# Kernel tuning notes

Measured on AMD Instinct MI355X. Metric: run time of the kernel, lower is better.

The kernel has to match this reference:

```python
import jax, jax.numpy as jnp
import numpy as np

N, M, C = 32768, 8192, 128
K = 3            # number of interpolation neighbors (PointNet++/RepSurf FP)
EPS_BN = 1e-5    # torch BatchNorm1d default eps
EPS_D = 1e-8     # RepSurf dist_recip eps


def setup_inputs() -> dict:
    key = jax.random.key(0)
    ks = jax.random.split(key, 16)
    s = 0.05
    inp = {
        "pos1": jax.random.normal(ks[0], (N, 3), jnp.float32),
        "pos2": jax.random.normal(ks[1], (M, 3), jnp.float32),
        "feat2": jax.random.normal(ks[2], (M, C), jnp.float32),
    }
    # MLP stack [128,128,128]: Linear + BatchNorm1d (gamma/beta) per layer
    for i in range(3):
        inp[f"W{i}"] = jax.random.normal(ks[3 + i], (C, C), jnp.float32) * s
        inp[f"b{i}"] = jnp.zeros((C,), jnp.float32)
        inp[f"g{i}"] = jnp.ones((C,), jnp.float32)
        inp[f"be{i}"] = jnp.zeros((C,), jnp.float32)
    return inp


def _lin_bn_relu(x, W, b, g, be):
    # Linear -> BatchNorm1d (training-mode batch stats, biased var) -> ReLU
    y = x @ W.T + b
    m = y.mean(axis=0)
    v = y.var(axis=0)
    return jax.nn.relu((y - m) * jax.lax.rsqrt(v + EPS_BN) * g + be)


def reference(pos1, pos2, feat2, W0, b0, g0, be0, W1, b1, g1, be1, W2, b2, g2, be2):
    # squared pairwise distances [N, M] (memory-bound: 1 GB fp32)
    d = ((pos1 ** 2).sum(-1, keepdims=True)
         + (pos2 ** 2).sum(-1)[None, :]
         - 2.0 * (pos1 @ pos2.T))
    neg_d, idx = jax.lax.top_k(-d, K)          # 3 nearest neighbors
    dk = jnp.maximum(-neg_d, 0.0)              # [N, K] squared dists
    w = 1.0 / (dk + EPS_D)
    w = w / w.sum(-1, keepdims=True)           # inverse-distance weights
    # gather neighbor features and interpolate: [N, K, C] -> [N, C]
    interp = jnp.einsum('nkc,nk->nc', feat2[idx], w)
    x = _lin_bn_relu(interp, W0, b0, g0, be0)
    x = _lin_bn_relu(x, W1, b1, g1, be1)
    x = _lin_bn_relu(x, W2, b2, g2, be2)
    return x
```

## Files before the change

### kernel.cpp

```cpp
#include <hip/hip_runtime.h>
#include <hip/hip_fp16.h>
#include <math.h>

#define NQ 32768
#define MC 8192
#define CC 128
#define EPS_BN 1e-5f
#define EPS_D  1e-8

#define DBL_BIG 1e300
#define IDX_BIG 0x7fffffff

#define QB  64
#define TB  256
#define NTIL 256
#define KMASK 0xFFFFE000u
#define IMASK 0x1FFFu
#define NSURV 24
#define KNN_B ((NQ / QB) * 2)
#define GEMM_B (NQ / 64)
#define NGRP 8

typedef __attribute__((ext_vector_type(8))) short bf16x8;
typedef __attribute__((ext_vector_type(8))) _Float16 half8;
typedef __attribute__((ext_vector_type(4))) float floatx4;
typedef unsigned short ushort_t;

__device__ __forceinline__ unsigned bf16pair(float a, float b) {
    unsigned ua = __float_as_uint(a); ua = (ua + 0x7FFFu + ((ua >> 16) & 1u)) >> 16;
    unsigned ub = __float_as_uint(b); ub = (ub + 0x7FFFu + ((ub >> 16) & 1u)) >> 16;
    return ua | (ub << 16);
}
__device__ __forceinline__ ushort_t bf16one(float a) {
    unsigned ua = __float_as_uint(a);
    return (ushort_t)((ua + 0x7FFFu + ((ua >> 16) & 1u)) >> 16);
}
__device__ __forceinline__ float bflo(unsigned u) { return __uint_as_float(u << 16); }
__device__ __forceinline__ float bfhi(unsigned u) { return __uint_as_float(u & 0xFFFF0000u); }

__device__ __forceinline__ void ins3(float& k0, float& k1, float& k2, float x) {
    const float n0 = fminf(k0, x);
    const float n1 = __builtin_amdgcn_fmed3f(k0, k1, x);
    const float n2 = __builtin_amdgcn_fmed3f(k1, k2, x);
    k0 = n0; k1 = n1; k2 = n2;
}

#define PK2(a, b) ((unsigned)__half_as_ushort(a) | ((unsigned)__half_as_ushort(b) << 16))

__global__ __launch_bounds__(TB) void pack_kernel(const float* __restrict__ pos2,
                                                  uint4* __restrict__ ptile) {
    const int c = blockIdx.x * TB + threadIdx.x;
    const float x = pos2[c * 3 + 0];
    const float y = pos2[c * 3 + 1];
    const float z = pos2[c * 3 + 2];
    const __half chx = __float2half(x); const float fchx = __half2float(chx);
    const __half chy = __float2half(y); const float fchy = __half2float(chy);
    const __half chz = __float2half(z); const float fchz = __half2float(chz);
    const __half clx = __float2half(x - fchx);
    const __half cly = __float2half(y - fchy);
    const __half clz = __float2half(z - fchz);
    const double X = (double)fchx + (double)__half2float(clx);
    const double Y = (double)fchy + (double)__half2float(cly);
    const double Z = (double)fchz + (double)__half2float(clz);
    const double hc = 0.5 * (X * X + Y * Y + Z * Z);
    const __half hchi = __float2half((float)hc);
    const __half hclo = __float2half((float)(hc - (double)__half2float(hchi)));
    const __half one = __float2half(1.0f);
    uint4 a0, a1;
    a0.x = PK2(chx, chy); a0.y = PK2(chz, clx); a0.z = PK2(cly, clz); a0.w = PK2(chx, chy);
    a1.x = PK2(chz, clx); a1.y = PK2(cly, clz); a1.z = PK2(hchi, hclo); a1.w = PK2(one, one);
    const int t = c >> 4, m = c & 15;
    ptile[(size_t)t * 32 + m]      = a0;
    ptile[(size_t)t * 32 + 16 + m] = a1;
}

__global__ __launch_bounds__(TB) void knn_kernel(const float* __restrict__ pos1,
                                                 const uint4* __restrict__ ptile,
                                                 unsigned* __restrict__ skeys,
                                                 const float* __restrict__ W0,
                                                 const float* __restrict__ W1,
                                                 const float* __restrict__ W2,
                                                 ushort_t* __restrict__ Wbf,
                                                 float* __restrict__ stats) {
    __shared__ __align__(16) ushort_t qext[QB][16];

    if (blockIdx.x >= KNN_B) {
        const int pb = blockIdx.x - KNN_B;
        const int f = pb * TB + threadIdx.x;
        const float* Ws[3] = {W0, W1, W2};
#pragma unroll
        for (int l = 0; l < 3; ++l) {
            const float4 v = ((const float4*)Ws[l])[f];
            unsigned* dst = (unsigned*)(Wbf + (size_t)l * CC * CC);
            dst[f * 2 + 0] = bf16pair(v.x, v.y);
            dst[f * 2 + 1] = bf16pair(v.z, v.w);
        }
        if (pb == 0)
            for (int i = threadIdx.x; i < 3 * NGRP * 256; i += TB) stats[i] = 0.f;
        return;
    }

    const int half = blockIdx.x & 1;
    const int bq   = blockIdx.x >> 1;

    if (threadIdx.x < QB) {
        const int qq = bq * QB + threadIdx.x;
        const float x = pos1[qq * 3 + 0];
        const float y = pos1[qq * 3 + 1];
        const float z = pos1[qq * 3 + 2];
        const __half phx = __float2half(x); const float fphx = __half2float(phx);
        const __half phy = __float2half(y); const float fphy = __half2float(phy);
        const __half phz = __float2half(z); const float fphz = __half2float(phz);
        const __half plx = __float2half(x - fphx);
        const __half ply = __float2half(y - fphy);
        const __half plz = __float2half(z - fphz);
        const double X = (double)fphx + (double)__half2float(plx);
        const double Y = (double)fphy + (double)__half2float(ply);
        const double Z = (double)fphz + (double)__half2float(plz);
        const double hp = 0.5 * (X * X + Y * Y + Z * Z);
        const __half hphi = __float2half((float)hp);
        const __half hplo = __float2half((float)(hp - (double)__half2float(hphi)));
        const ushort_t SG = 0x8000u;
        const ushort_t nx = (ushort_t)(__half_as_ushort(phx) ^ SG);
        const ushort_t ny = (ushort_t)(__half_as_ushort(phy) ^ SG);
        const ushort_t nz = (ushort_t)(__half_as_ushort(phz) ^ SG);
        const ushort_t mx = (ushort_t)(__half_as_ushort(plx) ^ SG);
        const ushort_t my = (ushort_t)(__half_as_ushort(ply) ^ SG);
        const ushort_t mz = (ushort_t)(__half_as_ushort(plz) ^ SG);
        const ushort_t on = __half_as_ushort(__float2half(1.0f));
        ushort_t* e = &qext[threadIdx.x][0];
        e[0] = nx; e[1] = ny; e[2] = nz; e[3] = nx; e[4]  = ny; e[5]  = nz;
        e[6] = mx; e[7] = my; e[8] = mz; e[9] = mx; e[10] = my; e[11] = mz;
        e[12] = on; e[13] = on;
        e[14] = __half_as_ushort(hphi); e[15] = __half_as_ushort(hplo);
    }
    __syncthreads();

    const int lane = threadIdx.x & 63;
    const int wv   = threadIdx.x >> 6;
    const int cc   = lane & 15;
    const int g    = lane >> 4;

    uint4 bqu = {0u, 0u, 0u, 0u};
    if (g < 2) bqu = *(const uint4*)&qext[wv * 16 + cc][g * 8];
    const half8 bqh = *(const half8*)&bqu;

    const uint4* lp = ptile + (size_t)(half * NTIL) * 32 + ((g & 1) * 16 + cc);
#define LD(t) lp[(size_t)(t) * 32]

    const float KINIT = __uint_as_float(0x7F000000u);
    float k0 = KINIT, k1 = KINIT, k2 = KINIT;
    unsigned j0 = (unsigned)(half * 4096 + g * 4 + 0);
    unsigned j1 = j0 + 1, j2 = j0 + 2, j3 = j0 + 3;
    const floatx4 zc = {0.f, 0.f, 0.f, 0.f};

#define KEYS(d) { \
        unsigned u0 = (__float_as_uint(d[0]) & KMASK) | (j0 & ~KMASK); \
        unsigned u1 = (__float_as_uint(d[1]) & KMASK) | (j1 & ~KMASK); \
        unsigned u2 = (__float_as_uint(d[2]) & KMASK) | (j2 & ~KMASK); \
        unsigned u3 = (__float_as_uint(d[3]) & KMASK) | (j3 & ~KMASK); \
        ins3(k0, k1, k2, __uint_as_float(u0)); \
        ins3(k0, k1, k2, __uint_as_float(u1)); \
        ins3(k0, k1, k2, __uint_as_float(u2)); \
        ins3(k0, k1, k2, __uint_as_float(u3)); \
        j0 += 16; j1 += 16; j2 += 16; j3 += 16; }

    uint4 afA = LD(0);
    uint4 afB = LD(1);
    for (int t = 0; t < NTIL; t += 2) {
        const uint4 nA = LD(t + 2);
        const floatx4 dA = __builtin_amdgcn_mfma_f32_16x16x32_f16(*(const half8*)&afA, bqh, zc, 0, 0, 0);
        KEYS(dA);
        const uint4 nB = LD(t + 3);
        const floatx4 dB = __builtin_amdgcn_mfma_f32_16x16x32_f16(*(const half8*)&afB, bqh, zc, 0, 0, 0);
        KEYS(dB);
        afA = nA; afB = nB;
    }
#undef LD
#undef KEYS

    {
        const int q = bq * QB + wv * 16 + cc;
        unsigned* dst = skeys + (size_t)q * NSURV + half * 12 + g * 3;
        dst[0] = __float_as_uint(k0);
        dst[1] = __float_as_uint(k1);
        dst[2] = __float_as_uint(k2);
    }
}

template <int MODE>
__global__ __launch_bounds__(256) void gemm_mfma(const void* __restrict__ Xsrc_,
                                                 const unsigned* __restrict__ skeys,
                                                 const float* __restrict__ pos1,
                                                 const float* __restrict__ pos2,
                                                 const float* __restrict__ statsIn,
                                                 const float* __restrict__ gIn,
                                                 const float* __restrict__ beIn,
                                                 const ushort_t* __restrict__ Wb,
                                                 const float* __restrict__ bias,
                                                 ushort_t* __restrict__ Y,
                                                 float* __restrict__ statsOut) {
    __shared__ __align__(16) short xa[64][136];
    __shared__ __align__(16) short wb[128][136];
    __shared__ float blk_s[CC], blk_q[CC];
    __shared__ float sc_l[CC], sh_l[CC];

    const int row0 = blockIdx.x * 64;

    if constexpr (MODE == 0) {
        const float* feat2 = (const float*)Xsrc_;
        __shared__ int   lidx[QB][3];
        __shared__ float lw[QB][3];
        {
            double* rrd = (double*)&xa[0][0];
            int*    rri = (int*)&wb[0][0];
            const int ql = threadIdx.x >> 2;
            const int pp = threadIdx.x & 3;
            const int qg = row0 + ql;
            const double qx = (double)pos1[qg * 3 + 0];
            const double qy = (double)pos1[qg * 3 + 1];
            const double qz = (double)pos1[qg * 3 + 2];
            double b0 = DBL_BIG, b1 = DBL_BIG, b2 = DBL_BIG;
            int    j0 = IDX_BIG, j1 = IDX_BIG, j2 = IDX_BIG;
            const uint2* kp = (const uint2*)(skeys + (size_t)qg * NSURV + pp * 6);
            const uint2 ka = kp[0], kb = kp[1], kc = kp[2];
            const unsigned ks[6] = {ka.x, ka.y, kb.x, kb.y, kc.x, kc.y};
#pragma unroll
            for (int u = 0; u < 6; ++u) {
                const int id = (int)(ks[u] & IMASK);
                const double x = (double)pos2[id * 3 + 0];
                const double y = (double)pos2[id * 3 + 1];
                const double z = (double)pos2[id * 3 + 2];
                const double ax = qx - x, ay = qy - y, az = qz - z;
                const double d = ax * ax + ay * ay + az * az;
                const bool l2 = (d < b2) || (d == b2 && id < j2);
                if (l2) {
                    const bool l1 = (d < b1) || (d == b1 && id < j1);
                    const bool l0 = (d < b0) || (d == b0 && id < j0);
                    b2 = l1 ? b1 : d;              j2 = l1 ? j1 : id;
                    b1 = l1 ? (l0 ? b0 : d) : b1;  j1 = l1 ? (l0 ? j0 : id) : j1;
                    b0 = l0 ? d : b0;              j0 = l0 ? id : j0;
                }
            }
            const int base = (ql * 4 + pp) * 3;
            rrd[base + 0] = b0; rri[base + 0] = j0;
            rrd[base + 1] = b1; rri[base + 1] = j1;
            rrd[base + 2] = b2; rri[base + 2] = j2;
            __syncthreads();
            if (threadIdx.x < QB) {
                const int qq = threadIdx.x;
                double c0 = DBL_BIG, c1 = DBL_BIG, c2 = DBL_BIG;
                int    i0 = IDX_BIG, i1 = IDX_BIG, i2 = IDX_BIG;
#pragma unroll
                for (int s = 0; s < 12; ++s) {
                    const double d = rrd[qq * 12 + s];
                    const int   id = rri[qq * 12 + s];
                    const bool l2 = (d < c2) || (d == c2 && id < i2);
                    if (l2) {
                        const bool l1 = (d < c1) || (d == c1 && id < i1);
                        const bool l0 = (d < c0) || (d == c0 && id < i0);
                        c2 = l1 ? c1 : d;              i2 = l1 ? i1 : id;
                        c1 = l1 ? (l0 ? c0 : d) : c1;  i1 = l1 ? (l0 ? i0 : id) : i1;
                        c0 = l0 ? d : c0;              i0 = l0 ? id : i0;
                    }
                }
                const double r0 = 1.0 / (c0 + EPS_D);
                const double r1 = 1.0 / (c1 + EPS_D);
                const double r2 = 1.0 / (c2 + EPS_D);
                const double inv = 1.0 / (r0 + r1 + r2);
                lidx[qq][0] = i0; lidx[qq][1] = i1; lidx[qq][2] = i2;
                lw[qq][0] = (float)(r0 * inv);
                lw[qq][1] = (float)(r1 * inv);
                lw[qq][2] = (float)(r2 * inv);
            }
            __syncthreads();
        }
        if (threadIdx.x < CC) { blk_s[threadIdx.x] = 0.f; blk_q[threadIdx.x] = 0.f; }
#pragma unroll
        for (int e = threadIdx.x; e < 64 * 32; e += 256) {
            const int r = e >> 5, c4 = e & 31;
            const int i0 = lidx[r][0], i1 = lidx[r][1], i2 = lidx[r][2];
            const float w0 = lw[r][0], w1 = lw[r][1], w2 = lw[r][2];
            const float4 f0 = *(const float4*)&feat2[(size_t)i0 * CC + c4 * 4];
            const float4 f1 = *(const float4*)&feat2[(size_t)i1 * CC + c4 * 4];
            const float4 f2 = *(const float4*)&feat2[(size_t)i2 * CC + c4 * 4];
            float4 v;
            v.x = w0 * f0.x + w1 * f1.x + w2 * f2.x;
            v.y = w0 * f0.y + w1 * f1.y + w2 * f2.y;
            v.z = w0 * f0.z + w1 * f1.z + w2 * f2.z;
            v.w = w0 * f0.w + w1 * f1.w + w2 * f2.w;
            unsigned* dst = (unsigned*)&xa[r][0];
            dst[c4 * 2 + 0] = bf16pair(v.x, v.y);
            dst[c4 * 2 + 1] = bf16pair(v.z, v.w);
        }
    } else {
        const ushort_t* Xbf = (const ushort_t*)Xsrc_;
        if (threadIdx.x < CC) {
            const int c = threadIdx.x;
            float s = 0.f, q = 0.f;
#pragma unroll
            for (int gr = 0; gr < NGRP; ++gr) {
                s += statsIn[gr * 256 + c];
                q += statsIn[gr * 256 + CC + c];
            }
            const float m = s * (1.f / (float)NQ);
            const float v = fmaf(-m, m, q * (1.f / (float)NQ));
            const float rstd = rsqrtf(v + EPS_BN);
            const float scl = gIn[c] * rstd;
            sc_l[c] = scl;
            sh_l[c] = fmaf(-m, scl, beIn[c]);
            blk_s[c] = 0.f; blk_q[c] = 0.f;
        }
        __syncthreads();
#pragma unroll
        for (int e = threadIdx.x; e < 64 * 16; e += 256) {
            const int r = e >> 4, c8 = e & 15;
            const uint4 u = *(const uint4*)&Xbf[(size_t)(row0 + r) * CC + c8 * 8];
            const float4 s0 = *(const float4*)&sc_l[c8 * 8];
            const float4 s1 = *(const float4*)&sc_l[c8 * 8 + 4];
            const float4 h0 = *(const float4*)&sh_l[c8 * 8];
            const float4 h1 = *(const float4*)&sh_l[c8 * 8 + 4];
            const float v0 = fmaxf(fmaf(bflo(u.x), s0.x, h0.x), 0.f);
            const float v1 = fmaxf(fmaf(bfhi(u.x), s0.y, h0.y), 0.f);
            const float v2 = fmaxf(fmaf(bflo(u.y), s0.z, h0.z), 0.f);
            const float v3 = fmaxf(fmaf(bfhi(u.y), s0.w, h0.w), 0.f);
            const float v4 = fmaxf(fmaf(bflo(u.z), s1.x, h1.x), 0.f);
            const float v5 = fmaxf(fmaf(bfhi(u.z), s1.y, h1.y), 0.f);
            const float v6 = fmaxf(fmaf(bflo(u.w), s1.z, h1.z), 0.f);
            const float v7 = fmaxf(fmaf(bfhi(u.w), s1.w, h1.w), 0.f);
            uint4 o;
            o.x = bf16pair(v0, v1); o.y = bf16pair(v2, v3);
            o.z = bf16pair(v4, v5); o.w = bf16pair(v6, v7);
            *(uint4*)&xa[r][c8 * 8] = o;
        }
    }
#pragma unroll
    for (int e = threadIdx.x; e < 128 * 16; e += 256) {
        const int co = e >> 4, seg = e & 15;
        *(float4*)&wb[co][seg * 8] = *(const float4*)&Wb[(size_t)co * CC + seg * 8];
    }
    __syncthreads();

    const int lane = threadIdx.x & 63;
    const int wv = threadIdx.x >> 6;
    const int nn = lane & 15;
    const int quad = lane >> 4;

    floatx4 acc[8] = {};

    const short* arow = &xa[wv * 16 + nn][0];
#pragma unroll
    for (int ks = 0; ks < 4; ++ks) {
        const bf16x8 a = *(const bf16x8*)(arow + ks * 32 + quad * 8);
#pragma unroll
        for (int ct = 0; ct < 8; ++ct) {
            const bf16x8 b = *(const bf16x8*)(&wb[ct * 16 + nn][0] + ks * 32 + quad * 8);
            acc[ct] = __builtin_amdgcn_mfma_f32_16x16x32_bf16(a, b, acc[ct], 0, 0, 0);
        }
    }

#pragma unroll
    for (int ct = 0; ct < 8; ++ct) {
        const float bv = bias[ct * 16 + nn];
        float s = 0.f, qv = 0.f;
#pragma unroll
        for (int r = 0; r < 4; ++r) {
            acc[ct][r] += bv;
            s += acc[ct][r];
            qv = fmaf(acc[ct][r], acc[ct][r], qv);
        }
#pragma unroll
        for (int r = 0; r < 4; ++r)
            Y[(size_t)(row0 + wv * 16 + quad * 4 + r) * CC + ct * 16 + nn] = bf16one(acc[ct][r]);
        s += __shfl_xor(s, 16, 64); s += __shfl_xor(s, 32, 64);
        qv += __shfl_xor(qv, 16, 64); qv += __shfl_xor(qv, 32, 64);
        if (quad == 0) {
            atomicAdd(&blk_s[ct * 16 + nn], s);
            atomicAdd(&blk_q[ct * 16 + nn], qv);
        }
    }
    __syncthreads();
    {
        const int ch = threadIdx.x;
        const float v = (ch < CC) ? blk_s[ch] : blk_q[ch - CC];
        atomicAdd(&statsOut[(blockIdx.x & (NGRP - 1)) * 256 + ch], v);
    }
}

__global__ __launch_bounds__(256) void bn_final(const ushort_t* __restrict__ Y,
                                                const float* __restrict__ statsIn,
                                                const float* __restrict__ g,
                                                const float* __restrict__ be,
                                                float* __restrict__ out) {
    __shared__ float sc_l[CC], sh_l[CC];
    if (threadIdx.x < CC) {
        const int c = threadIdx.x;
        float s = 0.f, q = 0.f;
#pragma unroll
        for (int gr = 0; gr < NGRP; ++gr) {
            s += statsIn[gr * 256 + c];
            q += statsIn[gr * 256 + CC + c];
        }
        const float m = s * (1.f / (float)NQ);
        const float v = fmaf(-m, m, q * (1.f / (float)NQ));
        const float rstd = rsqrtf(v + EPS_BN);
        const float scl = g[c] * rstd;
        sc_l[c] = scl;
        sh_l[c] = fmaf(-m, scl, be[c]);
    }
    __syncthreads();
    const int base = blockIdx.x * 1024 + threadIdx.x;
#pragma unroll
    for (int it = 0; it < 4; ++it) {
        const int i8 = base + it * 256;
        const int c8 = (i8 & 15) * 8;
        const uint4 u = *(const uint4*)&Y[(size_t)i8 * 8];
        const float4 s0 = *(const float4*)&sc_l[c8];
        const float4 s1 = *(const float4*)&sc_l[c8 + 4];
        const float4 h0 = *(const float4*)&sh_l[c8];
        const float4 h1 = *(const float4*)&sh_l[c8 + 4];
        float4 o0, o1;
        o0.x = fmaxf(fmaf(bflo(u.x), s0.x, h0.x), 0.f);
        o0.y = fmaxf(fmaf(bfhi(u.x), s0.y, h0.y), 0.f);
        o0.z = fmaxf(fmaf(bflo(u.y), s0.z, h0.z), 0.f);
        o0.w = fmaxf(fmaf(bfhi(u.y), s0.w, h0.w), 0.f);
        o1.x = fmaxf(fmaf(bflo(u.z), s1.x, h1.x), 0.f);
        o1.y = fmaxf(fmaf(bfhi(u.z), s1.y, h1.y), 0.f);
        o1.z = fmaxf(fmaf(bflo(u.w), s1.z, h1.z), 0.f);
        o1.w = fmaxf(fmaf(bfhi(u.w), s1.w, h1.w), 0.f);
        ((float4*)out)[i8 * 2 + 0] = o0;
        ((float4*)out)[i8 * 2 + 1] = o1;
    }
}

extern "C" void kernel_launch(void* const* d_in, const int* in_sizes, int n_in,
                              void* d_out, int out_size, void* d_ws, size_t ws_size,
                              hipStream_t stream) {
    (void)in_sizes; (void)n_in; (void)out_size; (void)ws_size;

    const float* pos1  = (const float*)d_in[0];
    const float* pos2  = (const float*)d_in[1];
    const float* feat2 = (const float*)d_in[2];
    const float* Wl[3]  = {(const float*)d_in[3], (const float*)d_in[7],  (const float*)d_in[11]};
    const float* bl[3]  = {(const float*)d_in[4], (const float*)d_in[8],  (const float*)d_in[12]};
    const float* gl[3]  = {(const float*)d_in[5], (const float*)d_in[9],  (const float*)d_in[13]};
    const float* bel[3] = {(const float*)d_in[6], (const float*)d_in[10], (const float*)d_in[14]};

    float* ws = (float*)d_ws;
    ushort_t* B0 = (ushort_t*)ws;
    ushort_t* B1 = B0 + (size_t)NQ * CC;
    unsigned* skeys = (unsigned*)(B1 + (size_t)NQ * CC);
    float* stats = (float*)(skeys + (size_t)NQ * NSURV);
    ushort_t* Wbf = (ushort_t*)(stats + 3 * NGRP * 256);
    uint4* ptile = (uint4*)(Wbf + 3 * CC * CC);

    float* st0 = stats + 0 * NGRP * 256;
    float* st1 = stats + 1 * NGRP * 256;
    float* st2 = stats + 2 * NGRP * 256;

    pack_kernel<<<MC / TB, TB, 0, stream>>>(pos2, ptile);
    knn_kernel<<<KNN_B + 16, TB, 0, stream>>>(pos1, ptile, skeys,
                                              Wl[0], Wl[1], Wl[2], Wbf, stats);
    gemm_mfma<0><<<GEMM_B, 256, 0, stream>>>(feat2, skeys, pos1, pos2,
                                             nullptr, nullptr, nullptr,
                                             Wbf + 0 * CC * CC, bl[0], B0, st0);
    gemm_mfma<1><<<GEMM_B, 256, 0, stream>>>(B0, nullptr, nullptr, nullptr,
                                             st0, gl[0], bel[0],
                                             Wbf + 1 * CC * CC, bl[1], B1, st1);
    gemm_mfma<1><<<GEMM_B, 256, 0, stream>>>(B1, nullptr, nullptr, nullptr,
                                             st1, gl[1], bel[1],
                                             Wbf + 2 * CC * CC, bl[2], B0, st2);
    bn_final<<<GEMM_B, 256, 0, stream>>>(B0, st2, gl[2], bel[2], (float*)d_out);
}
```

Measured before the change: 201.4 us.

## Switch KNN distance MFMA to 32x32x16 tiles and split candidates four ways

The brute-force KNN distance pass now uses 32x32x16 f16 MFMA instead of 16x16x32, so each wave covers 32 queries. Candidates are split into four pieces per query block, and each lane keeps four independent top-3 lists that are merged at the end. The point tile layout is rebuilt for 32-wide tiles, with zero padding added for the prefetch overrun. The survivor count per query doubles to 48, so the refinement step in the GEMM kernel reads and rechecks twice as many candidates in double precision. The aim is to raise MFMA throughput and shorten the serial insertion dependency chains, at the cost of more blocks, more survivor traffic and more refine work.

```diff
diff --git a/kernel.cpp b/kernel.cpp
--- a/kernel.cpp
+++ b/kernel.cpp
@@ -13,17 +13,19 @@
 
 #define QB  64
 #define TB  256
-#define NTIL 256
+#define PCE 2048
+#define NT  32
 #define KMASK 0xFFFFE000u
 #define IMASK 0x1FFFu
-#define NSURV 24
-#define KNN_B ((NQ / QB) * 2)
+#define NSURV 48
+#define KNN_B ((NQ / QB) * 4)
 #define GEMM_B (NQ / 64)
 #define NGRP 8
 
 typedef __attribute__((ext_vector_type(8))) short bf16x8;
 typedef __attribute__((ext_vector_type(8))) _Float16 half8;
 typedef __attribute__((ext_vector_type(4))) float floatx4;
+typedef __attribute__((ext_vector_type(16))) float floatx16;
 typedef unsigned short ushort_t;
 
 __device__ __forceinline__ unsigned bf16pair(float a, float b) {
@@ -69,9 +71,13 @@
     uint4 a0, a1;
     a0.x = PK2(chx, chy); a0.y = PK2(chz, clx); a0.z = PK2(cly, clz); a0.w = PK2(chx, chy);
     a1.x = PK2(chz, clx); a1.y = PK2(cly, clz); a1.z = PK2(hchi, hclo); a1.w = PK2(one, one);
-    const int t = c >> 4, m = c & 15;
-    ptile[(size_t)t * 32 + m]      = a0;
-    ptile[(size_t)t * 32 + 16 + m] = a1;
+    const int t = c >> 5, m = c & 31;
+    ptile[(size_t)t * 64 + m]      = a0;
+    ptile[(size_t)t * 64 + 32 + m] = a1;
+    if (blockIdx.x == 0 && threadIdx.x < 128) {
+        uint4 zf = {0u, 0u, 0u, 0u};
+        ptile[(size_t)256 * 64 + threadIdx.x] = zf;
+    }
 }
 
 __global__ __launch_bounds__(TB) void knn_kernel(const float* __restrict__ pos1,
@@ -100,8 +106,8 @@
         return;
     }
 
-    const int half = blockIdx.x & 1;
-    const int bq   = blockIdx.x >> 1;
+    const int piece = blockIdx.x & 3;
+    const int bq    = blockIdx.x >> 2;
 
     if (threadIdx.x < QB) {
         const int qq = bq * QB + threadIdx.x;
@@ -137,54 +143,69 @@
     __syncthreads();
 
     const int lane = threadIdx.x & 63;
-    const int wv   = threadIdx.x >> 6;
-    const int cc   = lane & 15;
-    const int g    = lane >> 4;
-
-    uint4 bqu = {0u, 0u, 0u, 0u};
-    if (g < 2) bqu = *(const uint4*)&qext[wv * 16 + cc][g * 8];
+    const int w    = threadIdx.x >> 6;
+    const int qt   = w >> 1;
+    const int wh   = w & 1;
+    const int col  = lane & 31;
+    const int h    = lane >> 5;
+
+    const uint4 bqu = *(const uint4*)&qext[qt * 32 + col][h * 8];
     const half8 bqh = *(const half8*)&bqu;
 
-    const uint4* lp = ptile + (size_t)(half * NTIL) * 32 + ((g & 1) * 16 + cc);
-#define LD(t) lp[(size_t)(t) * 32]
+    const int cw = piece * PCE + wh * 1024;
+    const uint4* lp = ptile + (size_t)(cw >> 5) * 64 + h * 32 + col;
+#define LD(t) lp[(size_t)(t) * 64]
 
     const float KINIT = __uint_as_float(0x7F000000u);
-    float k0 = KINIT, k1 = KINIT, k2 = KINIT;
-    unsigned j0 = (unsigned)(half * 4096 + g * 4 + 0);
-    unsigned j1 = j0 + 1, j2 = j0 + 2, j3 = j0 + 3;
-    const floatx4 zc = {0.f, 0.f, 0.f, 0.f};
-
+    float a0 = KINIT, a1 = KINIT, a2 = KINIT;
+    float b0 = KINIT, b1 = KINIT, b2 = KINIT;
+    float c0 = KINIT, c1 = KINIT, c2 = KINIT;
+    float d0 = KINIT, d1 = KINIT, d2 = KINIT;
+    unsigned ja = (unsigned)(cw + 4 * h + 0);
+    unsigned jb = (unsigned)(cw + 4 * h + 8);
+    unsigned jc = (unsigned)(cw + 4 * h + 16);
+    unsigned jd = (unsigned)(cw + 4 * h + 24);
+    const floatx16 zc = {0.f,0.f,0.f,0.f,0.f,0.f,0.f,0.f,0.f,0.f,0.f,0.f,0.f,0.f,0.f,0.f};
+
+#define KEY1(v, jj, K0, K1, K2) { \
+        const unsigned u_ = (__float_as_uint(v) & KMASK) | ((jj) & ~KMASK); \
+        ins3(K0, K1, K2, __uint_as_float(u_)); }
 #define KEYS(d) { \
-        unsigned u0 = (__float_as_uint(d[0]) & KMASK) | (j0 & ~KMASK); \
-        unsigned u1 = (__float_as_uint(d[1]) & KMASK) | (j1 & ~KMASK); \
-        unsigned u2 = (__float_as_uint(d[2]) & KMASK) | (j2 & ~KMASK); \
-        unsigned u3 = (__float_as_uint(d[3]) & KMASK) | (j3 & ~KMASK); \
-        ins3(k0, k1, k2, __uint_as_float(u0)); \
-        ins3(k0, k1, k2, __uint_as_float(u1)); \
-        ins3(k0, k1, k2, __uint_as_float(u2)); \
-        ins3(k0, k1, k2, __uint_as_float(u3)); \
-        j0 += 16; j1 += 16; j2 += 16; j3 += 16; }
-
-    uint4 afA = LD(0);
-    uint4 afB = LD(1);
-    for (int t = 0; t < NTIL; t += 2) {
-        const uint4 nA = LD(t + 2);
-        const floatx4 dA = __builtin_amdgcn_mfma_f32_16x16x32_f16(*(const half8*)&afA, bqh, zc, 0, 0, 0);
+        KEY1(d[0],  ja,     a0, a1, a2); KEY1(d[1],  ja + 1, a0, a1, a2); \
+        KEY1(d[2],  ja + 2, a0, a1, a2); KEY1(d[3],  ja + 3, a0, a1, a2); \
+        KEY1(d[4],  jb,     b0, b1, b2); KEY1(d[5],  jb + 1, b0, b1, b2); \
+        KEY1(d[6],  jb + 2, b0, b1, b2); KEY1(d[7],  jb + 3, b0, b1, b2); \
+        KEY1(d[8],  jc,     c0, c1, c2); KEY1(d[9],  jc + 1, c0, c1, c2); \
+        KEY1(d[10], jc + 2, c0, c1, c2); KEY1(d[11], jc + 3, c0, c1, c2); \
+        KEY1(d[12], jd,     d0, d1, d2); KEY1(d[13], jd + 1, d0, d1, d2); \
+        KEY1(d[14], jd + 2, d0, d1, d2); KEY1(d[15], jd + 3, d0, d1, d2); \
+        ja += 32; jb += 32; jc += 32; jd += 32; }
+
+    uint4 fA = LD(0);
+    uint4 fB = LD(1);
+    floatx16 dA = __builtin_amdgcn_mfma_f32_32x32x16_f16(*(const half8*)&fA, bqh, zc, 0, 0, 0);
+    for (int t = 0; t < NT; t += 2) {
+        fA = LD(t + 2);
+        const floatx16 dB = __builtin_amdgcn_mfma_f32_32x32x16_f16(*(const half8*)&fB, bqh, zc, 0, 0, 0);
         KEYS(dA);
-        const uint4 nB = LD(t + 3);
-        const floatx4 dB = __builtin_amdgcn_mfma_f32_16x16x32_f16(*(const half8*)&afB, bqh, zc, 0, 0, 0);
+        fB = LD(t + 3);
+        dA = __builtin_amdgcn_mfma_f32_32x32x16_f16(*(const half8*)&fA, bqh, zc, 0, 0, 0);
         KEYS(dB);
-        afA = nA; afB = nB;
     }
 #undef LD
 #undef KEYS
+#undef KEY1
+
+    ins3(a0, a1, a2, b0); ins3(a0, a1, a2, b1); ins3(a0, a1, a2, b2);
+    ins3(a0, a1, a2, c0); ins3(a0, a1, a2, c1); ins3(a0, a1, a2, c2);
+    ins3(a0, a1, a2, d0); ins3(a0, a1, a2, d1); ins3(a0, a1, a2, d2);
 
     {
-        const int q = bq * QB + wv * 16 + cc;
-        unsigned* dst = skeys + (size_t)q * NSURV + half * 12 + g * 3;
-        dst[0] = __float_as_uint(k0);
-        dst[1] = __float_as_uint(k1);
-        dst[2] = __float_as_uint(k2);
+        const int q = bq * QB + qt * 32 + col;
+        unsigned* dst = skeys + (size_t)q * NSURV + piece * 12 + wh * 6 + h * 3;
+        dst[0] = __float_as_uint(a0);
+        dst[1] = __float_as_uint(a1);
+        dst[2] = __float_as_uint(a2);
     }
 }
 
@@ -222,24 +243,27 @@
             const double qz = (double)pos1[qg * 3 + 2];
             double b0 = DBL_BIG, b1 = DBL_BIG, b2 = DBL_BIG;
             int    j0 = IDX_BIG, j1 = IDX_BIG, j2 = IDX_BIG;
-            const uint2* kp = (const uint2*)(skeys + (size_t)qg * NSURV + pp * 6);
-            const uint2 ka = kp[0], kb = kp[1], kc = kp[2];
-            const unsigned ks[6] = {ka.x, ka.y, kb.x, kb.y, kc.x, kc.y};
-#pragma unroll
-            for (int u = 0; u < 6; ++u) {
-                const int id = (int)(ks[u] & IMASK);
-                const double x = (double)pos2[id * 3 + 0];
-                const double y = (double)pos2[id * 3 + 1];
-                const double z = (double)pos2[id * 3 + 2];
-                const double ax = qx - x, ay = qy - y, az = qz - z;
-                const double d = ax * ax + ay * ay + az * az;
-                const bool l2 = (d < b2) || (d == b2 && id < j2);
-                if (l2) {
-                    const bool l1 = (d < b1) || (d == b1 && id < j1);
-                    const bool l0 = (d < b0) || (d == b0 && id < j0);
-                    b2 = l1 ? b1 : d;              j2 = l1 ? j1 : id;
-                    b1 = l1 ? (l0 ? b0 : d) : b1;  j1 = l1 ? (l0 ? j0 : id) : j1;
-                    b0 = l0 ? d : b0;              j0 = l0 ? id : j0;
+            const uint4* kp = (const uint4*)(skeys + (size_t)qg * NSURV + pp * 12);
+#pragma unroll
+            for (int gi = 0; gi < 3; ++gi) {
+                const uint4 kk = kp[gi];
+                const unsigned ks[4] = {kk.x, kk.y, kk.z, kk.w};
+#pragma unroll
+                for (int u = 0; u < 4; ++u) {
+                    const int id = (int)(ks[u] & IMASK);
+                    const double x = (double)pos2[id * 3 + 0];
+                    const double y = (double)pos2[id * 3 + 1];
+                    const double z = (double)pos2[id * 3 + 2];
+                    const double ax = qx - x, ay = qy - y, az = qz - z;
+                    const double d = ax * ax + ay * ay + az * az;
+                    const bool l2 = (d < b2) || (d == b2 && id < j2);
+                    if (l2) {
+                        const bool l1 = (d < b1) || (d == b1 && id < j1);
+                        const bool l0 = (d < b0) || (d == b0 && id < j0);
+                        b2 = l1 ? b1 : d;              j2 = l1 ? j1 : id;
+                        b1 = l1 ? (l0 ? b0 : d) : b1;  j1 = l1 ? (l0 ? j0 : id) : j1;
+                        b0 = l0 ? d : b0;              j0 = l0 ? id : j0;
+                    }
                 }
             }
             const int base = (ql * 4 + pp) * 3;
```

New measurement: 193.0 us. 1.04x faster.
